# Performance work log

Hardware: AMD Instinct MI355X
Metric: run time of the kernel (lower is better)

## Reference

```python
import jax, jax.numpy as jnp
import numpy as np

N = 12288          # neuron_count (nodes.shape[0])
R = 1024           # retina_output_size[1]
B = 32             # batch
N_LAYERS = 4       # CONNECTOME_LAYER_NUMBER
DENSITY = 0.05     # adjacency (connectome) sparsity
N_VISUAL = 2048    # neurons flagged 'visual'
N_RATIONAL = 64    # neurons flagged 'rational'


def setup_inputs() -> dict:
    key = jax.random.key(0)
    k_x, k_ret, k_sh, k_adj, k_rat, k_vis, k_ridx = jax.random.split(key, 7)

    x = jax.random.normal(k_x, (B, R), dtype=jnp.float32)

    # Retina layer: Linear(R -> N, bias=False); only rows at visual indices nonzero.
    vis_idx = jax.random.permutation(k_vis, N)[:N_VISUAL]
    vis_mask = jnp.zeros((N,), jnp.float32).at[vis_idx].set(1.0)
    W_retina = jax.random.normal(k_ret, (N, R), dtype=jnp.float32) * vis_mask[:, None]

    # Shared connectome weights: rand(N,N) masked by transposed adjacency != 0.
    adj = jax.random.bernoulli(k_adj, DENSITY, (N, N)).astype(jnp.float32)
    W_shared = jax.random.uniform(k_sh, (N, N), dtype=jnp.float32) * adj

    # Rational layer: Linear(N -> 2); only columns at rational indices nonzero.
    rat_idx = jax.random.permutation(k_ridx, N)[:N_RATIONAL]
    rat_mask = jnp.zeros((N,), jnp.float32).at[rat_idx].set(1.0)
    W_rational = jax.random.normal(k_rat, (2, N), dtype=jnp.float32) * rat_mask[None, :]

    return {"x": x, "W_retina": W_retina, "W_shared": W_shared,
            "W_rational": W_rational, "n_layers": N_LAYERS}


def reference(x, W_retina, W_shared, W_rational, n_layers):
    # retina: out = x @ W_retina^T   -> [B, N]
    out = jnp.einsum('br,nr->bn', x, W_retina)
    # repeated shared-weight Linear (bias-free): out = out @ W_shared^T
    for _ in range(n_layers):
        out = jnp.einsum('bn,mn->bm', out, W_shared)
    # rational readout: [B, 2]
    return jnp.einsum('bn,on->bo', out, W_rational)
```

## Files before the change

### kernel.cpp

```cpp
#include <hip/hip_runtime.h>
#include <cstddef>

#define NN 12288
#define RR 1024
#define BB 32

#define MSEGS 64
#define MROWS (NN / MSEGS)
#define JBLK (NN / 1024)
#define CAP 32

#define PSEGS 256
#define PJ (NN / PSEGS)

typedef float vfloat4 __attribute__((ext_vector_type(4)));

__global__ __launch_bounds__(256) void skip_fold_kernel(
    const float* __restrict__ W, const float* __restrict__ hin,
    float* __restrict__ hpart)
{
    const int t   = threadIdx.x;
    const int jb  = blockIdx.x;
    const int seg = blockIdx.y;
    const int j   = jb * 1024 + t * 4;
    const int m0  = seg * MROWS;

    __shared__ float h0s[MROWS];
    __shared__ float h1s[MROWS];
    if (t < MROWS) {
        h0s[t] = hin[m0 + t];
        h1s[t] = hin[NN + m0 + t];
    }
    __syncthreads();

    float a00 = 0.f, a01 = 0.f, a02 = 0.f, a03 = 0.f;
    float a10 = 0.f, a11 = 0.f, a12 = 0.f, a13 = 0.f;

    const float4* Wp = (const float4*)(W + (size_t)m0 * NN + j);
    for (int i = 0; i < MROWS; ++i) {
        const float hm0 = h0s[i];
        const float hm1 = h1s[i];
        if (hm0 != 0.f || hm1 != 0.f) {
            const float4 w = *Wp;
            a00 = fmaf(hm0, w.x, a00); a01 = fmaf(hm0, w.y, a01);
            a02 = fmaf(hm0, w.z, a02); a03 = fmaf(hm0, w.w, a03);
            a10 = fmaf(hm1, w.x, a10); a11 = fmaf(hm1, w.y, a11);
            a12 = fmaf(hm1, w.z, a12); a13 = fmaf(hm1, w.w, a13);
        }
        Wp += NN / 4;
    }

    float* d0 = hpart + ((size_t)seg * 2) * NN + j;
    d0[0] = a00; d0[1] = a01; d0[2] = a02; d0[3] = a03;
    float* d1 = d0 + NN;
    d1[0] = a10; d1[1] = a11; d1[2] = a12; d1[3] = a13;
}

__global__ __launch_bounds__(256) void build_kernel(
    const float* __restrict__ W, float* __restrict__ sval,
    unsigned char* __restrict__ sidx, unsigned char* __restrict__ scnt)
{
    const int t   = threadIdx.x;
    const int jb  = blockIdx.x;
    const int seg = blockIdx.y;
    const int j   = jb * 1024 + t * 4;
    const int m0  = seg * MROWS;

    const vfloat4* Wp = (const vfloat4*)(W + (size_t)m0 * NN + j);
    float*         vb = sval + ((size_t)seg * CAP) * NN + j;
    unsigned char* ib = sidx + ((size_t)seg * CAP) * NN + j;

    int c0 = 0, c1 = 0, c2 = 0, c3 = 0;
    for (int i = 0; i < MROWS; ++i) {
        const vfloat4 w = __builtin_nontemporal_load(Wp);
        Wp += NN / 4;
        const unsigned char li = (unsigned char)i;
        if (w.x != 0.f) { if (c0 < CAP) { vb[(size_t)c0 * NN + 0] = w.x; ib[(size_t)c0 * NN + 0] = li; } c0++; }
        if (w.y != 0.f) { if (c1 < CAP) { vb[(size_t)c1 * NN + 1] = w.y; ib[(size_t)c1 * NN + 1] = li; } c1++; }
        if (w.z != 0.f) { if (c2 < CAP) { vb[(size_t)c2 * NN + 2] = w.z; ib[(size_t)c2 * NN + 2] = li; } c2++; }
        if (w.w != 0.f) { if (c3 < CAP) { vb[(size_t)c3 * NN + 3] = w.w; ib[(size_t)c3 * NN + 3] = li; } c3++; }
    }
    uchar4 cn;
    cn.x = (unsigned char)(c0 < CAP ? c0 : CAP);
    cn.y = (unsigned char)(c1 < CAP ? c1 : CAP);
    cn.z = (unsigned char)(c2 < CAP ? c2 : CAP);
    cn.w = (unsigned char)(c3 < CAP ? c3 : CAP);
    *(uchar4*)(scnt + (size_t)seg * NN + j) = cn;
}

__global__ __launch_bounds__(256) void sfold_kernel(
    const float* __restrict__ sval, const unsigned char* __restrict__ sidx,
    const unsigned char* __restrict__ scnt,
    const float* __restrict__ hin, float* __restrict__ hpart)
{
    const int seg = blockIdx.y;
    const int j   = blockIdx.x * 256 + threadIdx.x;
    const int m0  = seg * MROWS;

    __shared__ float2 hs[MROWS];
    if (threadIdx.x < MROWS)
        hs[threadIdx.x] = make_float2(hin[m0 + threadIdx.x], hin[NN + m0 + threadIdx.x]);
    __syncthreads();

    const int cnt = scnt[(size_t)seg * NN + j];
    const float*         vp = sval + ((size_t)seg * CAP) * NN + j;
    const unsigned char* ip = sidx + ((size_t)seg * CAP) * NN + j;

    float a0 = 0.f, a1 = 0.f;
    for (int k = 0; k < cnt; ++k) {
        const float v = vp[(size_t)k * NN];
        const int   m = ip[(size_t)k * NN];
        const float2 h = hs[m];
        a0 = fmaf(v, h.x, a0);
        a1 = fmaf(v, h.y, a1);
    }
    hpart[((size_t)seg * 2) * NN + j]     = a0;
    hpart[((size_t)seg * 2 + 1) * NN + j] = a1;
}

__global__ __launch_bounds__(256) void reduce_h_kernel(
    const float* __restrict__ hpart, float* __restrict__ hout)
{
    const int idx = blockIdx.x * 256 + threadIdx.x;
    float s = 0.f;
    for (int seg = 0; seg < MSEGS; ++seg)
        s += hpart[(size_t)seg * 2 * NN + idx];
    hout[idx] = s;
}

__global__ __launch_bounds__(256) void retina_fold_kernel(
    const float* __restrict__ Wret, const float* __restrict__ h,
    float* __restrict__ ppart)
{
    const int seg = blockIdx.x;
    const int t   = threadIdx.x;
    const int j0  = seg * PJ;

    __shared__ float h0s[PJ];
    __shared__ float h1s[PJ];
    if (t < PJ) {
        h0s[t] = h[j0 + t];
        h1s[t] = h[NN + j0 + t];
    }
    __syncthreads();

    const int r = t * 4;
    float a00 = 0.f, a01 = 0.f, a02 = 0.f, a03 = 0.f;
    float a10 = 0.f, a11 = 0.f, a12 = 0.f, a13 = 0.f;

    const float4* Wp = (const float4*)(Wret + (size_t)j0 * RR + r);
    #pragma unroll 4
    for (int i = 0; i < PJ; ++i) {
        const float4 w = *Wp;
        Wp += RR / 4;
        const float h0 = h0s[i];
        const float h1 = h1s[i];
        a00 = fmaf(h0, w.x, a00); a01 = fmaf(h0, w.y, a01);
        a02 = fmaf(h0, w.z, a02); a03 = fmaf(h0, w.w, a03);
        a10 = fmaf(h1, w.x, a10); a11 = fmaf(h1, w.y, a11);
        a12 = fmaf(h1, w.z, a12); a13 = fmaf(h1, w.w, a13);
    }

    float* d0 = ppart + ((size_t)seg * 2) * RR + r;
    d0[0] = a00; d0[1] = a01; d0[2] = a02; d0[3] = a03;
    float* d1 = d0 + RR;
    d1[0] = a10; d1[1] = a11; d1[2] = a12; d1[3] = a13;
}

__global__ __launch_bounds__(256) void reduce_p_kernel(
    const float* __restrict__ ppart, float* __restrict__ p)
{
    const int idx = blockIdx.x * 256 + threadIdx.x;
    float s = 0.f;
    for (int seg = 0; seg < PSEGS; ++seg)
        s += ppart[(size_t)seg * 2 * RR + idx];
    p[idx] = s;
}

__global__ __launch_bounds__(64) void final_kernel(
    const float* __restrict__ x, const float* __restrict__ p,
    float* __restrict__ out)
{
    const int t = threadIdx.x;
    const int b = t >> 1;
    const int o = t & 1;
    const float4* xp = (const float4*)(x + (size_t)b * RR);
    const float4* pp = (const float4*)(p + (size_t)o * RR);
    float s = 0.f;
    for (int i = 0; i < RR / 4; ++i) {
        const float4 xv = xp[i];
        const float4 pv = pp[i];
        s = fmaf(xv.x, pv.x, s);
        s = fmaf(xv.y, pv.y, s);
        s = fmaf(xv.z, pv.z, s);
        s = fmaf(xv.w, pv.w, s);
    }
    out[b * 2 + o] = s;
}

extern "C" void kernel_launch(void* const* d_in, const int* in_sizes, int n_in,
                              void* d_out, int out_size, void* d_ws, size_t ws_size,
                              hipStream_t stream) {
    const float* x    = (const float*)d_in[0];
    const float* Wret = (const float*)d_in[1];
    const float* Ws   = (const float*)d_in[2];
    const float* Wrat = (const float*)d_in[3];

    char* ws = (char*)d_ws;
    float*         sval  = (float*)(ws + 0);
    unsigned char* sidx  = (unsigned char*)(ws + 100663296);
    unsigned char* scnt  = (unsigned char*)(ws + 125829120);
    float*         hpart = (float*)(ws + 126615552);
    float*         ppart = (float*)(ws + 132907008);
    float*         hA    = (float*)(ws + 135004160);
    float*         hB    = (float*)(ws + 135102464);
    float*         p     = (float*)(ws + 135200768);

    const dim3 denseGrid(JBLK, MSEGS);
    const dim3 sfoldGrid(NN / 256, MSEGS);

    build_kernel<<<denseGrid, 256, 0, stream>>>(Ws, sval, sidx, scnt);

    skip_fold_kernel<<<denseGrid, 256, 0, stream>>>(Ws, Wrat, hpart);
    reduce_h_kernel<<<(2 * NN) / 256, 256, 0, stream>>>(hpart, hA);

    sfold_kernel<<<sfoldGrid, 256, 0, stream>>>(sval, sidx, scnt, hA, hpart);
    reduce_h_kernel<<<(2 * NN) / 256, 256, 0, stream>>>(hpart, hB);

    sfold_kernel<<<sfoldGrid, 256, 0, stream>>>(sval, sidx, scnt, hB, hpart);
    reduce_h_kernel<<<(2 * NN) / 256, 256, 0, stream>>>(hpart, hA);

    sfold_kernel<<<sfoldGrid, 256, 0, stream>>>(sval, sidx, scnt, hA, hpart);
    reduce_h_kernel<<<(2 * NN) / 256, 256, 0, stream>>>(hpart, hB);

    retina_fold_kernel<<<PSEGS, 256, 0, stream>>>(Wret, hB, ppart);
    reduce_p_kernel<<<(2 * RR) / 256, 256, 0, stream>>>(ppart, p);

    final_kernel<<<1, 64, 0, stream>>>(x, p, (float*)d_out);
}
```

Before: 1.031 ms.

## Pack row index into mantissa low bits and store sparse entries contiguously per column

The sparse build now writes each column's nonzeros contiguously (CAP floats per column) and stores the 8-bit row index in the low mantissa byte of each value, which removes the separate index array. The fold kernel reads these with float4 vector loads, and the first dense skip-fold pass over W_shared is replaced by a sparse fold. This reduces build-write and fold-read traffic and drops one full dense read of the weight matrix. In exchange, weights lose 8 mantissa bits of precision, the CAP overflow guard is removed so a column segment with more than CAP nonzeros would write out of bounds, and per-thread strided contiguous writes may coalesce poorly during the build.

After: 1.047 ms. No clear change (+1.6%).

```diff
diff --git a/kernel.cpp b/kernel.cpp
--- a/kernel.cpp
+++ b/kernel.cpp
@@ -15,9 +15,9 @@
 
 typedef float vfloat4 __attribute__((ext_vector_type(4)));
 
-__global__ __launch_bounds__(256) void skip_fold_kernel(
-    const float* __restrict__ W, const float* __restrict__ hin,
-    float* __restrict__ hpart)
+__global__ __launch_bounds__(256) void build_kernel(
+    const float* __restrict__ W, float* __restrict__ sval,
+    unsigned char* __restrict__ scnt)
 {
     const int t   = threadIdx.x;
     const int jb  = blockIdx.x;
@@ -25,72 +25,29 @@
     const int j   = jb * 1024 + t * 4;
     const int m0  = seg * MROWS;
 
-    __shared__ float h0s[MROWS];
-    __shared__ float h1s[MROWS];
-    if (t < MROWS) {
-        h0s[t] = hin[m0 + t];
-        h1s[t] = hin[NN + m0 + t];
-    }
-    __syncthreads();
-
-    float a00 = 0.f, a01 = 0.f, a02 = 0.f, a03 = 0.f;
-    float a10 = 0.f, a11 = 0.f, a12 = 0.f, a13 = 0.f;
-
-    const float4* Wp = (const float4*)(W + (size_t)m0 * NN + j);
-    for (int i = 0; i < MROWS; ++i) {
-        const float hm0 = h0s[i];
-        const float hm1 = h1s[i];
-        if (hm0 != 0.f || hm1 != 0.f) {
-            const float4 w = *Wp;
-            a00 = fmaf(hm0, w.x, a00); a01 = fmaf(hm0, w.y, a01);
-            a02 = fmaf(hm0, w.z, a02); a03 = fmaf(hm0, w.w, a03);
-            a10 = fmaf(hm1, w.x, a10); a11 = fmaf(hm1, w.y, a11);
-            a12 = fmaf(hm1, w.z, a12); a13 = fmaf(hm1, w.w, a13);
-        }
-        Wp += NN / 4;
-    }
-
-    float* d0 = hpart + ((size_t)seg * 2) * NN + j;
-    d0[0] = a00; d0[1] = a01; d0[2] = a02; d0[3] = a03;
-    float* d1 = d0 + NN;
-    d1[0] = a10; d1[1] = a11; d1[2] = a12; d1[3] = a13;
-}
-
-__global__ __launch_bounds__(256) void build_kernel(
-    const float* __restrict__ W, float* __restrict__ sval,
-    unsigned char* __restrict__ sidx, unsigned char* __restrict__ scnt)
-{
-    const int t   = threadIdx.x;
-    const int jb  = blockIdx.x;
-    const int seg = blockIdx.y;
-    const int j   = jb * 1024 + t * 4;
-    const int m0  = seg * MROWS;
-
     const vfloat4* Wp = (const vfloat4*)(W + (size_t)m0 * NN + j);
-    float*         vb = sval + ((size_t)seg * CAP) * NN + j;
-    unsigned char* ib = sidx + ((size_t)seg * CAP) * NN + j;
+    float* v0 = sval + ((size_t)seg * NN + j) * CAP;
+    float* v1 = v0 + CAP;
+    float* v2 = v0 + 2 * CAP;
+    float* v3 = v0 + 3 * CAP;
 
     int c0 = 0, c1 = 0, c2 = 0, c3 = 0;
     for (int i = 0; i < MROWS; ++i) {
         const vfloat4 w = __builtin_nontemporal_load(Wp);
         Wp += NN / 4;
-        const unsigned char li = (unsigned char)i;
-        if (w.x != 0.f) { if (c0 < CAP) { vb[(size_t)c0 * NN + 0] = w.x; ib[(size_t)c0 * NN + 0] = li; } c0++; }
-        if (w.y != 0.f) { if (c1 < CAP) { vb[(size_t)c1 * NN + 1] = w.y; ib[(size_t)c1 * NN + 1] = li; } c1++; }
-        if (w.z != 0.f) { if (c2 < CAP) { vb[(size_t)c2 * NN + 2] = w.z; ib[(size_t)c2 * NN + 2] = li; } c2++; }
-        if (w.w != 0.f) { if (c3 < CAP) { vb[(size_t)c3 * NN + 3] = w.w; ib[(size_t)c3 * NN + 3] = li; } c3++; }
+        if (w.x != 0.f) { unsigned int b = __float_as_uint(w.x); v0[c0++] = __uint_as_float((b & 0xFFFFFF00u) | (unsigned)i); }
+        if (w.y != 0.f) { unsigned int b = __float_as_uint(w.y); v1[c1++] = __uint_as_float((b & 0xFFFFFF00u) | (unsigned)i); }
+        if (w.z != 0.f) { unsigned int b = __float_as_uint(w.z); v2[c2++] = __uint_as_float((b & 0xFFFFFF00u) | (unsigned)i); }
+        if (w.w != 0.f) { unsigned int b = __float_as_uint(w.w); v3[c3++] = __uint_as_float((b & 0xFFFFFF00u) | (unsigned)i); }
     }
     uchar4 cn;
-    cn.x = (unsigned char)(c0 < CAP ? c0 : CAP);
-    cn.y = (unsigned char)(c1 < CAP ? c1 : CAP);
-    cn.z = (unsigned char)(c2 < CAP ? c2 : CAP);
-    cn.w = (unsigned char)(c3 < CAP ? c3 : CAP);
+    cn.x = (unsigned char)c0; cn.y = (unsigned char)c1;
+    cn.z = (unsigned char)c2; cn.w = (unsigned char)c3;
     *(uchar4*)(scnt + (size_t)seg * NN + j) = cn;
 }
 
 __global__ __launch_bounds__(256) void sfold_kernel(
-    const float* __restrict__ sval, const unsigned char* __restrict__ sidx,
-    const unsigned char* __restrict__ scnt,
+    const float* __restrict__ sval, const unsigned char* __restrict__ scnt,
     const float* __restrict__ hin, float* __restrict__ hpart)
 {
     const int seg = blockIdx.y;
@@ -103,16 +60,24 @@
     __syncthreads();
 
     const int cnt = scnt[(size_t)seg * NN + j];
-    const float*         vp = sval + ((size_t)seg * CAP) * NN + j;
-    const unsigned char* ip = sidx + ((size_t)seg * CAP) * NN + j;
+    const float4* vp = (const float4*)(sval + ((size_t)seg * NN + j) * CAP);
 
     float a0 = 0.f, a1 = 0.f;
-    for (int k = 0; k < cnt; ++k) {
-        const float v = vp[(size_t)k * NN];
-        const int   m = ip[(size_t)k * NN];
-        const float2 h = hs[m];
-        a0 = fmaf(v, h.x, a0);
-        a1 = fmaf(v, h.y, a1);
+    const int nq = (cnt + 3) >> 2;
+    for (int q = 0; q < nq; ++q) {
+        const float4 v4 = vp[q];
+        const int k = q * 4;
+        #pragma unroll
+        for (int u = 0; u < 4; ++u) {
+            const float vv = (u == 0) ? v4.x : (u == 1) ? v4.y : (u == 2) ? v4.z : v4.w;
+            if (k + u < cnt) {
+                const unsigned int b = __float_as_uint(vv);
+                const float v = __uint_as_float(b & 0xFFFFFF00u);
+                const float2 h = hs[b & 0xFFu];
+                a0 = fmaf(v, h.x, a0);
+                a1 = fmaf(v, h.y, a1);
+            }
+        }
     }
     hpart[((size_t)seg * 2) * NN + j]     = a0;
     hpart[((size_t)seg * 2 + 1) * NN + j] = a1;
@@ -208,29 +173,28 @@
 
     char* ws = (char*)d_ws;
     float*         sval  = (float*)(ws + 0);
-    unsigned char* sidx  = (unsigned char*)(ws + 100663296);
-    unsigned char* scnt  = (unsigned char*)(ws + 125829120);
-    float*         hpart = (float*)(ws + 126615552);
-    float*         ppart = (float*)(ws + 132907008);
-    float*         hA    = (float*)(ws + 135004160);
-    float*         hB    = (float*)(ws + 135102464);
-    float*         p     = (float*)(ws + 135200768);
-
-    const dim3 denseGrid(JBLK, MSEGS);
+    unsigned char* scnt  = (unsigned char*)(ws + 100663296);
+    float*         hpart = (float*)(ws + 101449728);
+    float*         ppart = (float*)(ws + 107741184);
+    float*         hA    = (float*)(ws + 109838336);
+    float*         hB    = (float*)(ws + 109936640);
+    float*         p     = (float*)(ws + 110034944);
+
+    const dim3 buildGrid(JBLK, MSEGS);
     const dim3 sfoldGrid(NN / 256, MSEGS);
 
-    build_kernel<<<denseGrid, 256, 0, stream>>>(Ws, sval, sidx, scnt);
-
-    skip_fold_kernel<<<denseGrid, 256, 0, stream>>>(Ws, Wrat, hpart);
+    build_kernel<<<buildGrid, 256, 0, stream>>>(Ws, sval, scnt);
+
+    sfold_kernel<<<sfoldGrid, 256, 0, stream>>>(sval, scnt, Wrat, hpart);
     reduce_h_kernel<<<(2 * NN) / 256, 256, 0, stream>>>(hpart, hA);
 
-    sfold_kernel<<<sfoldGrid, 256, 0, stream>>>(sval, sidx, scnt, hA, hpart);
+    sfold_kernel<<<sfoldGrid, 256, 0, stream>>>(sval, scnt, hA, hpart);
     reduce_h_kernel<<<(2 * NN) / 256, 256, 0, stream>>>(hpart, hB);
 
-    sfold_kernel<<<sfoldGrid, 256, 0, stream>>>(sval, sidx, scnt, hB, hpart);
+    sfold_kernel<<<sfoldGrid, 256, 0, stream>>>(sval, scnt, hB, hpart);
     reduce_h_kernel<<<(2 * NN) / 256, 256, 0, stream>>>(hpart, hA);
 
-    sfold_kernel<<<sfoldGrid, 256, 0, stream>>>(sval, sidx, scnt, hA, hpart);
+    sfold_kernel<<<sfoldGrid, 256, 0, stream>>>(sval, scnt, hA, hpart);
     reduce_h_kernel<<<(2 * NN) / 256, 256, 0, stream>>>(hpart, hB);
 
     retina_fold_kernel<<<PSEGS, 256, 0, stream>>>(Wret, hB, ppart);
```
